# Kernel tuning notes

Hardware: AMD Instinct MI355X
Metric: run time of the kernel (lower is better)

The kernel has to match this reference:

```python
import jax, jax.numpy as jnp
import numpy as np

TOP_K = 2


def setup_inputs() -> dict:
    key = jax.random.key(0)
    ks = jax.random.split(key, 5)
    B, S, H, E, I = 2, 1024, 1024, 16, 1024
    scale = 1.0 / np.sqrt(H)
    return {
        "hidden_states": jax.random.normal(ks[0], (B, S, H), dtype=jnp.float32),
        "router_w": jax.random.normal(ks[1], (E, H), dtype=jnp.float32) * scale,   # nn.Linear(H,E).weight
        "gate_w": jax.random.normal(ks[2], (E, I, H), dtype=jnp.float32) * scale,  # per-expert Linear(H,I).weight
        "up_w": jax.random.normal(ks[3], (E, I, H), dtype=jnp.float32) * scale,
        "down_w": jax.random.normal(ks[4], (E, H, I), dtype=jnp.float32) * (1.0 / np.sqrt(I)),
    }


def reference(hidden_states, router_w, gate_w, up_w, down_w):
    orig_shape = hidden_states.shape
    x = hidden_states.reshape(-1, orig_shape[-1])  # [T, H]
    T = x.shape[0]
    E = router_w.shape[0]

    # Router: sigmoid -> top-k -> normalize
    logits = jnp.einsum("th,eh->te", x, router_w)           # [T, E]
    scores = jax.nn.sigmoid(logits)
    weights, indices = jax.lax.top_k(scores, TOP_K)         # [T, K]
    weights = weights / (weights.sum(axis=-1, keepdims=True) + 1e-20)

    # Dense per-token-per-expert combine weight (0 for unrouted pairs) ==
    # exact math of the torch gather/index_add loop.
    w_full = jnp.zeros((T, E), dtype=x.dtype).at[
        jnp.arange(T)[:, None], indices
    ].add(weights)                                          # [T, E]

    # Expert MLPs (SwiGLU) computed for all experts, zero-weighted combine.
    g = jax.nn.silu(jnp.einsum("th,eih->tei", x, gate_w))   # [T, E, I]
    u = jnp.einsum("th,eih->tei", x, up_w)                  # [T, E, I]
    out = jnp.einsum("te,tei,ehi->th", w_full, g * u, down_w)  # [T, H]
    return out.reshape(orig_shape)
```

## Files before the change

### kernel.cpp

```cpp
#include <hip/hip_runtime.h>
#include <stdint.h>

#define T_TOK 2048
#define H_DIM 1024
#define E_NUM 16
#define I_DIM 1024
#define TOTAL_ROWS (2 * T_TOK)
#define CPAD 16

typedef short bf16x8 __attribute__((ext_vector_type(8)));
typedef float f32x4 __attribute__((ext_vector_type(4)));

__device__ __forceinline__ void async_copy16(const void* g, void* l) {
  __builtin_amdgcn_global_load_lds(
      (const __attribute__((address_space(1))) void*)g,
      (__attribute__((address_space(3))) void*)l, 16, 0, 0);
}

__device__ __forceinline__ uint32_t f2bf(float f) {
  uint32_t u = __float_as_uint(f);
  return (u + 0x7FFFu + ((u >> 16) & 1u)) >> 16;
}
__device__ __forceinline__ uint32_t pk2bf(float lo, float hi) {
  return f2bf(lo) | (f2bf(hi) << 16);
}

__global__ __launch_bounds__(256) void router_kernel(
    const float* __restrict__ x, const float* __restrict__ rw,
    uint16_t* __restrict__ xbf, int* __restrict__ counts,
    int* __restrict__ tokens, float* __restrict__ wts) {
  const int t = blockIdx.x * 4 + (threadIdx.x >> 6);
  const int lane = threadIdx.x & 63;

  float4 xv[4];
  float acc[E_NUM];
#pragma unroll
  for (int e = 0; e < E_NUM; ++e) acc[e] = 0.f;

#pragma unroll
  for (int rep = 0; rep < 4; ++rep) {
    const int h0 = rep * 256 + lane * 4;
    xv[rep] = *(const float4*)(x + (size_t)t * H_DIM + h0);
    uint2 p;
    p.x = pk2bf(xv[rep].x, xv[rep].y);
    p.y = pk2bf(xv[rep].z, xv[rep].w);
    *(uint2*)(xbf + (size_t)t * H_DIM + h0) = p;
  }

#pragma unroll
  for (int e = 0; e < E_NUM; ++e) {
#pragma unroll
    for (int rep = 0; rep < 4; ++rep) {
      const float4 rv = *(const float4*)(rw + (size_t)e * H_DIM + rep * 256 + lane * 4);
      acc[e] += xv[rep].x * rv.x + xv[rep].y * rv.y + xv[rep].z * rv.z +
                xv[rep].w * rv.w;
    }
  }

#pragma unroll
  for (int e = 0; e < E_NUM; ++e) {
    float v = acc[e];
#pragma unroll
    for (int off = 32; off > 0; off >>= 1) v += __shfl_xor(v, off);
    acc[e] = v;
  }

  if (lane < 2) {
    float s[E_NUM];
#pragma unroll
    for (int e = 0; e < E_NUM; ++e) s[e] = 1.f / (1.f + expf(-acc[e]));
    int i1 = 0;
    float v1 = s[0];
#pragma unroll
    for (int e = 1; e < E_NUM; ++e)
      if (s[e] > v1) { v1 = s[e]; i1 = e; }
    int i2 = -1;
    float v2 = -1.f;
#pragma unroll
    for (int e = 0; e < E_NUM; ++e)
      if (e != i1 && s[e] > v2) { v2 = s[e]; i2 = e; }
    const float inv = 1.f / (v1 + v2 + 1e-20f);
    const int pe = (lane == 0) ? i1 : i2;
    const float pw = ((lane == 0) ? v1 : v2) * inv;
    const int slot = atomicAdd(&counts[pe * CPAD], 1);
    tokens[pe * T_TOK + slot] = t;
    wts[pe * T_TOK + slot] = pw;
  }
}

__global__ void offsets_kernel(const int* __restrict__ counts,
                               int* __restrict__ offsets) {
  if (threadIdx.x == 0) {
    int a = 0;
    for (int e = 0; e < E_NUM; ++e) {
      offsets[e] = a;
      a += counts[e * CPAD];
    }
    offsets[E_NUM] = a;
  }
}


__global__ __launch_bounds__(256, 3) void gemm1_kernel(
    const uint16_t* __restrict__ xbf, const float* __restrict__ gate,
    const float* __restrict__ up, const int* __restrict__ counts,
    const int* __restrict__ offsets, const int* __restrict__ tokens,
    const float* __restrict__ wts, uint16_t* __restrict__ hbuf) {
  const int e = blockIdx.z;
  const int count = counts[e * CPAD];
  const int m0 = blockIdx.y * 128;
  if (m0 >= count) return;
  const int n0 = blockIdx.x * 32;

  __shared__ __align__(16) uint16_t As[2][128 * 64];
  __shared__ __align__(16) uint16_t Bgs[2][32 * 64];
  __shared__ __align__(16) uint16_t Bus[2][32 * 64];
  __shared__ int tok_s[128];
  __shared__ float wt_s[128];

  const int tid = threadIdx.x;
  if (tid < 128) {
    const int slot = m0 + tid;
    int tk = 0;
    float w = 0.f;
    if (slot < count) {
      tk = tokens[e * T_TOK + slot];
      w = wts[e * T_TOK + slot];
    }
    tok_s[tid] = tk;
    wt_s[tid] = w;
  }
  __syncthreads();

  const uint16_t* a_g[4];
  int a_c[4];
#pragma unroll
  for (int j = 0; j < 4; ++j) {
    const int c = j * 256 + tid;
    const int m = c >> 3;
    const int kq = (c & 7) ^ (m & 7);
    a_g[j] = xbf + (size_t)tok_s[m] * H_DIM + kq * 8;
    a_c[j] = c * 8;
  }
  const int bm = tid >> 3;
  const int bkq = (tid & 7) ^ (bm & 7);
  const float* g_g = gate + ((size_t)e * I_DIM + n0 + bm) * H_DIM + bkq * 8;
  const float* u_g = up + ((size_t)e * I_DIM + n0 + bm) * H_DIM + bkq * 8;
  const int b_c = tid * 8;

  const int wave = tid >> 6, lane = tid & 63;
  const int wm = wave * 32;
  const int lc = lane & 15, lq = lane >> 4;
  const int l7 = lc & 7;

  f32x4 accg[2][2], accu[2][2];
  const f32x4 zero4 = {0.f, 0.f, 0.f, 0.f};
#pragma unroll
  for (int i = 0; i < 2; ++i)
#pragma unroll
    for (int j = 0; j < 2; ++j) {
      accg[i][j] = zero4;
      accu[i][j] = zero4;
    }

  int am[2], bn[2];
#pragma unroll
  for (int i = 0; i < 2; ++i) am[i] = (wm + i * 16 + lc) * 64;
#pragma unroll
  for (int i = 0; i < 2; ++i) bn[i] = (i * 16 + lc) * 64;

#pragma unroll
  for (int j = 0; j < 4; ++j) async_copy16(a_g[j], &As[0][a_c[j]]);
  float4 g0 = *(const float4*)g_g;
  float4 g1 = *(const float4*)(g_g + 4);
  float4 u0 = *(const float4*)u_g;
  float4 u1 = *(const float4*)(u_g + 4);
  {
    uint4 p;
    p.x = pk2bf(g0.x, g0.y);
    p.y = pk2bf(g0.z, g0.w);
    p.z = pk2bf(g1.x, g1.y);
    p.w = pk2bf(g1.z, g1.w);
    *(uint4*)&Bgs[0][b_c] = p;
    p.x = pk2bf(u0.x, u0.y);
    p.y = pk2bf(u0.z, u0.w);
    p.z = pk2bf(u1.x, u1.y);
    p.w = pk2bf(u1.z, u1.w);
    *(uint4*)&Bus[0][b_c] = p;
  }
  __syncthreads();

  int cur = 0;
  for (int k0 = 0; k0 < H_DIM; k0 += 64) {
    const int nxt = k0 + 64;
    const bool more = (nxt < H_DIM);
    if (more) {
#pragma unroll
      for (int j = 0; j < 4; ++j)
        async_copy16(a_g[j] + nxt, &As[cur ^ 1][a_c[j]]);
      g0 = *(const float4*)(g_g + nxt);
      g1 = *(const float4*)(g_g + nxt + 4);
      u0 = *(const float4*)(u_g + nxt);
      u1 = *(const float4*)(u_g + nxt + 4);
    }

#pragma unroll
    for (int ks = 0; ks < 2; ++ks) {
      const int kswz = ((ks * 4 + lq) ^ l7) * 8;
      bf16x8 af[2], bg[2], bu[2];
#pragma unroll
      for (int i = 0; i < 2; ++i)
        af[i] = *(const bf16x8*)&As[cur][am[i] + kswz];
#pragma unroll
      for (int i = 0; i < 2; ++i) {
        bg[i] = *(const bf16x8*)&Bgs[cur][bn[i] + kswz];
        bu[i] = *(const bf16x8*)&Bus[cur][bn[i] + kswz];
      }
#pragma unroll
      for (int im = 0; im < 2; ++im)
#pragma unroll
        for (int in = 0; in < 2; ++in) {
          accg[im][in] = __builtin_amdgcn_mfma_f32_16x16x32_bf16(
              af[im], bg[in], accg[im][in], 0, 0, 0);
          accu[im][in] = __builtin_amdgcn_mfma_f32_16x16x32_bf16(
              af[im], bu[in], accu[im][in], 0, 0, 0);
        }
    }

    if (more) {
      uint4 p;
      p.x = pk2bf(g0.x, g0.y);
      p.y = pk2bf(g0.z, g0.w);
      p.z = pk2bf(g1.x, g1.y);
      p.w = pk2bf(g1.z, g1.w);
      *(uint4*)&Bgs[cur ^ 1][b_c] = p;
      p.x = pk2bf(u0.x, u0.y);
      p.y = pk2bf(u0.z, u0.w);
      p.z = pk2bf(u1.x, u1.y);
      p.w = pk2bf(u1.z, u1.w);
      *(uint4*)&Bus[cur ^ 1][b_c] = p;
      __syncthreads();
      cur ^= 1;
    }
  }

  const int off_e = offsets[e];
#pragma unroll
  for (int im = 0; im < 2; ++im) {
#pragma unroll
    for (int r = 0; r < 4; ++r) {
      const int row = wm + im * 16 + lq * 4 + r;
      const int slot = m0 + row;
      if (slot < count) {
        const float w = wt_s[row];
        uint16_t* hrow = hbuf + (size_t)(off_e + slot) * I_DIM + n0;
#pragma unroll
        for (int in = 0; in < 2; ++in) {
          const float g = accg[im][in][r];
          const float u = accu[im][in][r];
          const float hv = g / (1.f + __expf(-g)) * u * w;
          hrow[in * 16 + lc] = (uint16_t)f2bf(hv);
        }
      }
    }
  }
}

__global__ __launch_bounds__(256, 3) void gemm2_kernel(
    const uint16_t* __restrict__ hbuf, const float* __restrict__ down,
    const int* __restrict__ counts, const int* __restrict__ offsets,
    const int* __restrict__ tokens, float* __restrict__ out) {
  const int e = blockIdx.z;
  const int count = counts[e * CPAD];
  const int m0 = blockIdx.y * 128;
  if (m0 >= count) return;
  const int n0 = blockIdx.x * 32;

  __shared__ __align__(16) uint16_t As[2][128 * 64];
  __shared__ __align__(16) uint16_t Bs[2][32 * 64];
  __shared__ int tok_s[128];

  const int tid = threadIdx.x;
  const int off_e = offsets[e];
  if (tid < 128) {
    const int slot = m0 + tid;
    tok_s[tid] = (slot < count) ? tokens[e * T_TOK + slot] : 0;
  }

  const uint16_t* a_g[4];
  int a_c[4];
#pragma unroll
  for (int j = 0; j < 4; ++j) {
    const int c = j * 256 + tid;
    const int m = c >> 3;
    const int kq = (c & 7) ^ (m & 7);
    int r = off_e + m0 + m;
    if (r > TOTAL_ROWS - 1) r = TOTAL_ROWS - 1;
    a_g[j] = hbuf + (size_t)r * I_DIM + kq * 8;
    a_c[j] = c * 8;
  }
  const int bm = tid >> 3;
  const int bkq = (tid & 7) ^ (bm & 7);
  const float* d_g = down + ((size_t)e * H_DIM + n0 + bm) * I_DIM + bkq * 8;
  const int b_c = tid * 8;

  const int wave = tid >> 6, lane = tid & 63;
  const int wm = wave * 32;
  const int lc = lane & 15, lq = lane >> 4;
  const int l7 = lc & 7;

  f32x4 acc[2][2];
  const f32x4 zero4 = {0.f, 0.f, 0.f, 0.f};
#pragma unroll
  for (int i = 0; i < 2; ++i)
#pragma unroll
    for (int j = 0; j < 2; ++j) acc[i][j] = zero4;

  int am[2], bn[2];
#pragma unroll
  for (int i = 0; i < 2; ++i) am[i] = (wm + i * 16 + lc) * 64;
#pragma unroll
  for (int i = 0; i < 2; ++i) bn[i] = (i * 16 + lc) * 64;

#pragma unroll
  for (int j = 0; j < 4; ++j) async_copy16(a_g[j], &As[0][a_c[j]]);
  float4 d0 = *(const float4*)d_g;
  float4 d1 = *(const float4*)(d_g + 4);
  {
    uint4 p;
    p.x = pk2bf(d0.x, d0.y);
    p.y = pk2bf(d0.z, d0.w);
    p.z = pk2bf(d1.x, d1.y);
    p.w = pk2bf(d1.z, d1.w);
    *(uint4*)&Bs[0][b_c] = p;
  }
  __syncthreads();

  int cur = 0;
  for (int k0 = 0; k0 < I_DIM; k0 += 64) {
    const int nxt = k0 + 64;
    const bool more = (nxt < I_DIM);
    if (more) {
#pragma unroll
      for (int j = 0; j < 4; ++j)
        async_copy16(a_g[j] + nxt, &As[cur ^ 1][a_c[j]]);
      d0 = *(const float4*)(d_g + nxt);
      d1 = *(const float4*)(d_g + nxt + 4);
    }

#pragma unroll
    for (int ks = 0; ks < 2; ++ks) {
      const int kswz = ((ks * 4 + lq) ^ l7) * 8;
      bf16x8 af[2], bf[2];
#pragma unroll
      for (int i = 0; i < 2; ++i)
        af[i] = *(const bf16x8*)&As[cur][am[i] + kswz];
#pragma unroll
      for (int i = 0; i < 2; ++i)
        bf[i] = *(const bf16x8*)&Bs[cur][bn[i] + kswz];
#pragma unroll
      for (int im = 0; im < 2; ++im)
#pragma unroll
        for (int in = 0; in < 2; ++in)
          acc[im][in] = __builtin_amdgcn_mfma_f32_16x16x32_bf16(
              af[im], bf[in], acc[im][in], 0, 0, 0);
    }

    if (more) {
      uint4 p;
      p.x = pk2bf(d0.x, d0.y);
      p.y = pk2bf(d0.z, d0.w);
      p.z = pk2bf(d1.x, d1.y);
      p.w = pk2bf(d1.z, d1.w);
      *(uint4*)&Bs[cur ^ 1][b_c] = p;
      __syncthreads();
      cur ^= 1;
    }
  }

#pragma unroll
  for (int im = 0; im < 2; ++im) {
#pragma unroll
    for (int r = 0; r < 4; ++r) {
      const int row = wm + im * 16 + lq * 4 + r;
      const int slot = m0 + row;
      if (slot < count) {
        float* orow = out + (size_t)tok_s[row] * H_DIM + n0;
#pragma unroll
        for (int in = 0; in < 2; ++in)
          atomicAdd(orow + in * 16 + lc, acc[im][in][r]);
      }
    }
  }
}

extern "C" void kernel_launch(void* const* d_in, const int* in_sizes, int n_in,
                              void* d_out, int out_size, void* d_ws,
                              size_t ws_size, hipStream_t stream) {
  const float* x = (const float*)d_in[0];
  const float* rw = (const float*)d_in[1];
  const float* gate = (const float*)d_in[2];
  const float* up = (const float*)d_in[3];
  const float* down = (const float*)d_in[4];
  float* out = (float*)d_out;

  uint8_t* ws = (uint8_t*)d_ws;
  int* counts = (int*)ws;
  int* offsets = (int*)(ws + 2048);
  int* tokens = (int*)(ws + 4096);
  float* wts = (float*)(ws + 4096 + 131072);
  uint16_t* xbf = (uint16_t*)(ws + 4096 + 262144);
  uint16_t* hbuf = (uint16_t*)(ws + 4096 + 262144 + 4194304);

  hipMemsetAsync(counts, 0, 2048, stream);
  hipMemsetAsync(out, 0, (size_t)out_size * sizeof(float), stream);

  router_kernel<<<512, 256, 0, stream>>>(x, rw, xbf, counts, tokens, wts);
  offsets_kernel<<<1, 64, 0, stream>>>(counts, offsets);
  gemm1_kernel<<<dim3(32, 16, 16), 256, 0, stream>>>(
      xbf, gate, up, counts, offsets, tokens, wts, hbuf);
  gemm2_kernel<<<dim3(32, 16, 16), 256, 0, stream>>>(hbuf, down, counts,
                                                     offsets, tokens, out);
}
```

Before: 299.5 us.

## Pre-convert expert weights to swizzled bf16 tiles before grouped GEMMs

Adds a prep phase to the router kernel that converts gate, up and down weights from fp32 to bf16 in a tiled, XOR-swizzled layout in workspace. The GEMM kernels then stream the bf16 tiles with async LDS copies and use wider 64-column N tiles, so expert weights no longer need in-kernel fp32 loading and conversion. The cost is an extra full pass over all weights each call (reading 192MB of fp32 and writing 96MB of bf16). It also needs about 100MB more workspace and falls back to the old kernels when that space is not available.

```diff
diff --git a/kernel.cpp b/kernel.cpp
--- a/kernel.cpp
+++ b/kernel.cpp
@@ -25,66 +25,114 @@
   return f2bf(lo) | (f2bf(hi) << 16);
 }
 
-__global__ __launch_bounds__(256) void router_kernel(
+#define WS_COUNTS 0
+#define WS_OFFSETS 2048
+#define WS_TOKENS 4096
+#define WS_WTS (4096 + 131072)
+#define WS_XBF (4096 + 262144)
+#define WS_HBUF (WS_XBF + 4194304)
+#define WS_GBUF (WS_HBUF + 8388608)
+#define WS_UBUF (WS_GBUF + 33554432)
+#define WS_DBUF (WS_UBUF + 33554432)
+#define WS_NEED (WS_DBUF + 33554432)
+
+__global__ __launch_bounds__(256) void router_prep_kernel(
     const float* __restrict__ x, const float* __restrict__ rw,
-    uint16_t* __restrict__ xbf, int* __restrict__ counts,
-    int* __restrict__ tokens, float* __restrict__ wts) {
-  const int t = blockIdx.x * 4 + (threadIdx.x >> 6);
-  const int lane = threadIdx.x & 63;
-
-  float4 xv[4];
-  float acc[E_NUM];
-#pragma unroll
-  for (int e = 0; e < E_NUM; ++e) acc[e] = 0.f;
-
-#pragma unroll
-  for (int rep = 0; rep < 4; ++rep) {
-    const int h0 = rep * 256 + lane * 4;
-    xv[rep] = *(const float4*)(x + (size_t)t * H_DIM + h0);
-    uint2 p;
-    p.x = pk2bf(xv[rep].x, xv[rep].y);
-    p.y = pk2bf(xv[rep].z, xv[rep].w);
-    *(uint2*)(xbf + (size_t)t * H_DIM + h0) = p;
-  }
-
-#pragma unroll
-  for (int e = 0; e < E_NUM; ++e) {
+    const float* __restrict__ gate, const float* __restrict__ up,
+    const float* __restrict__ down, uint16_t* __restrict__ xbf,
+    int* __restrict__ counts, int* __restrict__ tokens,
+    float* __restrict__ wts, uint16_t* __restrict__ gbuf,
+    uint16_t* __restrict__ ubuf, uint16_t* __restrict__ dbuf) {
+  const int bid = blockIdx.x;
+  const int tid = threadIdx.x;
+
+  if (bid < 512) {
+    const int t = bid * 4 + (tid >> 6);
+    const int lane = tid & 63;
+
+    float4 xv[4];
+    float acc[E_NUM];
+#pragma unroll
+    for (int e = 0; e < E_NUM; ++e) acc[e] = 0.f;
+
 #pragma unroll
     for (int rep = 0; rep < 4; ++rep) {
-      const float4 rv = *(const float4*)(rw + (size_t)e * H_DIM + rep * 256 + lane * 4);
-      acc[e] += xv[rep].x * rv.x + xv[rep].y * rv.y + xv[rep].z * rv.z +
-                xv[rep].w * rv.w;
-    }
-  }
-
-#pragma unroll
-  for (int e = 0; e < E_NUM; ++e) {
-    float v = acc[e];
-#pragma unroll
-    for (int off = 32; off > 0; off >>= 1) v += __shfl_xor(v, off);
-    acc[e] = v;
-  }
-
-  if (lane < 2) {
-    float s[E_NUM];
-#pragma unroll
-    for (int e = 0; e < E_NUM; ++e) s[e] = 1.f / (1.f + expf(-acc[e]));
-    int i1 = 0;
-    float v1 = s[0];
-#pragma unroll
-    for (int e = 1; e < E_NUM; ++e)
-      if (s[e] > v1) { v1 = s[e]; i1 = e; }
-    int i2 = -1;
-    float v2 = -1.f;
-#pragma unroll
-    for (int e = 0; e < E_NUM; ++e)
-      if (e != i1 && s[e] > v2) { v2 = s[e]; i2 = e; }
-    const float inv = 1.f / (v1 + v2 + 1e-20f);
-    const int pe = (lane == 0) ? i1 : i2;
-    const float pw = ((lane == 0) ? v1 : v2) * inv;
-    const int slot = atomicAdd(&counts[pe * CPAD], 1);
-    tokens[pe * T_TOK + slot] = t;
-    wts[pe * T_TOK + slot] = pw;
+      const int h0 = rep * 256 + lane * 4;
+      xv[rep] = *(const float4*)(x + (size_t)t * H_DIM + h0);
+      uint2 p;
+      p.x = pk2bf(xv[rep].x, xv[rep].y);
+      p.y = pk2bf(xv[rep].z, xv[rep].w);
+      *(uint2*)(xbf + (size_t)t * H_DIM + h0) = p;
+    }
+
+#pragma unroll
+    for (int e = 0; e < E_NUM; ++e) {
+#pragma unroll
+      for (int rep = 0; rep < 4; ++rep) {
+        const float4 rv =
+            *(const float4*)(rw + (size_t)e * H_DIM + rep * 256 + lane * 4);
+        acc[e] += xv[rep].x * rv.x + xv[rep].y * rv.y + xv[rep].z * rv.z +
+                  xv[rep].w * rv.w;
+      }
+    }
+
+#pragma unroll
+    for (int e = 0; e < E_NUM; ++e) {
+      float v = acc[e];
+#pragma unroll
+      for (int off = 32; off > 0; off >>= 1) v += __shfl_xor(v, off);
+      acc[e] = v;
+    }
+
+    if (lane < 2) {
+      float s[E_NUM];
+#pragma unroll
+      for (int e = 0; e < E_NUM; ++e) s[e] = 1.f / (1.f + expf(-acc[e]));
+      int i1 = 0;
+      float v1 = s[0];
+#pragma unroll
+      for (int e = 1; e < E_NUM; ++e)
+        if (s[e] > v1) { v1 = s[e]; i1 = e; }
+      int i2 = -1;
+      float v2 = -1.f;
+#pragma unroll
+      for (int e = 0; e < E_NUM; ++e)
+        if (e != i1 && s[e] > v2) { v2 = s[e]; i2 = e; }
+      const float inv = 1.f / (v1 + v2 + 1e-20f);
+      const int pe = (lane == 0) ? i1 : i2;
+      const float pw = ((lane == 0) ? v1 : v2) * inv;
+      const int slot = atomicAdd(&counts[pe * CPAD], 1);
+      tokens[pe * T_TOK + slot] = t;
+      wts[pe * T_TOK + slot] = pw;
+    }
+    return;
+  }
+
+  const int tt = bid - 512;
+  const int mat = tt >> 12;
+  const int r = tt & 4095;
+  const int e = r >> 8;
+  const int nt = (r >> 4) & 15;
+  const int kt = r & 15;
+  const float* W = (mat == 0) ? gate : (mat == 1) ? up : down;
+  uint16_t* D = (mat == 0) ? gbuf : (mat == 1) ? ubuf : dbuf;
+  const float* src = W + ((size_t)e * 1024 + (size_t)nt * 64) * 1024 + kt * 64;
+  uint16_t* dst = D + ((size_t)((e * 16 + nt) * 16 + kt)) * 4096;
+
+#pragma unroll
+  for (int h = 0; h < 2; ++h) {
+    const int c = tid + h * 256;
+    const int m = c >> 3;
+    const int kq = (c & 7) ^ (m & 7);
+    const float* s = src + (size_t)m * 1024 + kq * 8;
+    const float4 a = *(const float4*)s;
+    const float4 b = *(const float4*)(s + 4);
+    uint4 p;
+    p.x = pk2bf(a.x, a.y);
+    p.y = pk2bf(a.z, a.w);
+    p.z = pk2bf(b.x, b.y);
+    p.w = pk2bf(b.z, b.w);
+    *(uint4*)(dst + (size_t)c * 8) = p;
   }
 }
 
@@ -100,8 +148,262 @@
   }
 }
 
-
-__global__ __launch_bounds__(256, 3) void gemm1_kernel(
+__global__ __launch_bounds__(256, 2) void gemm1_kernel(
+    const uint16_t* __restrict__ xbf, const uint16_t* __restrict__ gbuf,
+    const uint16_t* __restrict__ ubuf, const int* __restrict__ counts,
+    const int* __restrict__ offsets, const int* __restrict__ tokens,
+    const float* __restrict__ wts, uint16_t* __restrict__ hbuf) {
+  const int e = blockIdx.z;
+  const int count = counts[e * CPAD];
+  const int m0 = blockIdx.y * 128;
+  if (m0 >= count) return;
+  const int n0t = blockIdx.x;
+
+  __shared__ __align__(16) uint16_t As[2][128 * 64];
+  __shared__ __align__(16) uint16_t Bgs[2][64 * 64];
+  __shared__ __align__(16) uint16_t Bus[2][64 * 64];
+  __shared__ int tok_s[128];
+  __shared__ float wt_s[128];
+
+  const int tid = threadIdx.x;
+  if (tid < 128) {
+    const int slot = m0 + tid;
+    int tk = 0;
+    float w = 0.f;
+    if (slot < count) {
+      tk = tokens[e * T_TOK + slot];
+      w = wts[e * T_TOK + slot];
+    }
+    tok_s[tid] = tk;
+    wt_s[tid] = w;
+  }
+  __syncthreads();
+
+  const uint16_t* a_g[4];
+  int a_c[4];
+#pragma unroll
+  for (int j = 0; j < 4; ++j) {
+    const int c = j * 256 + tid;
+    const int m = c >> 3;
+    const int kq = (c & 7) ^ (m & 7);
+    a_g[j] = xbf + (size_t)tok_s[m] * H_DIM + kq * 8;
+    a_c[j] = c * 8;
+  }
+  const uint16_t* g_g = gbuf + (size_t)((e * 16 + n0t) * 16) * 4096;
+  const uint16_t* u_g = ubuf + (size_t)((e * 16 + n0t) * 16) * 4096;
+  const int bc0 = tid * 8, bc1 = (tid + 256) * 8;
+
+  const int wave = tid >> 6, lane = tid & 63;
+  const int wm = wave * 32;
+  const int lc = lane & 15, lq = lane >> 4;
+  const int l7 = lc & 7;
+
+  f32x4 accg[2][4], accu[2][4];
+  const f32x4 zero4 = {0.f, 0.f, 0.f, 0.f};
+#pragma unroll
+  for (int i = 0; i < 2; ++i)
+#pragma unroll
+    for (int j = 0; j < 4; ++j) {
+      accg[i][j] = zero4;
+      accu[i][j] = zero4;
+    }
+
+  int am[2], bn[4];
+#pragma unroll
+  for (int i = 0; i < 2; ++i) am[i] = (wm + i * 16 + lc) * 64;
+#pragma unroll
+  for (int i = 0; i < 4; ++i) bn[i] = (i * 16 + lc) * 64;
+
+#pragma unroll
+  for (int j = 0; j < 4; ++j) async_copy16(a_g[j], &As[0][a_c[j]]);
+  async_copy16(g_g + bc0, &Bgs[0][bc0]);
+  async_copy16(g_g + bc1, &Bgs[0][bc1]);
+  async_copy16(u_g + bc0, &Bus[0][bc0]);
+  async_copy16(u_g + bc1, &Bus[0][bc1]);
+  __syncthreads();
+
+  int cur = 0;
+  for (int kt = 0; kt < 16; ++kt) {
+    const bool more = (kt < 15);
+    if (more) {
+      const int ko = (kt + 1) * 64;
+      const int bo = (kt + 1) * 4096;
+      const int nb = cur ^ 1;
+#pragma unroll
+      for (int j = 0; j < 4; ++j) async_copy16(a_g[j] + ko, &As[nb][a_c[j]]);
+      async_copy16(g_g + bo + bc0, &Bgs[nb][bc0]);
+      async_copy16(g_g + bo + bc1, &Bgs[nb][bc1]);
+      async_copy16(u_g + bo + bc0, &Bus[nb][bc0]);
+      async_copy16(u_g + bo + bc1, &Bus[nb][bc1]);
+    }
+
+#pragma unroll
+    for (int ks = 0; ks < 2; ++ks) {
+      const int kswz = ((ks * 4 + lq) ^ l7) * 8;
+      bf16x8 af[2], bg[4], bu[4];
+#pragma unroll
+      for (int i = 0; i < 2; ++i)
+        af[i] = *(const bf16x8*)&As[cur][am[i] + kswz];
+#pragma unroll
+      for (int i = 0; i < 4; ++i) {
+        bg[i] = *(const bf16x8*)&Bgs[cur][bn[i] + kswz];
+        bu[i] = *(const bf16x8*)&Bus[cur][bn[i] + kswz];
+      }
+#pragma unroll
+      for (int im = 0; im < 2; ++im)
+#pragma unroll
+        for (int in = 0; in < 4; ++in) {
+          accg[im][in] = __builtin_amdgcn_mfma_f32_16x16x32_bf16(
+              af[im], bg[in], accg[im][in], 0, 0, 0);
+          accu[im][in] = __builtin_amdgcn_mfma_f32_16x16x32_bf16(
+              af[im], bu[in], accu[im][in], 0, 0, 0);
+        }
+    }
+
+    if (more) {
+      __syncthreads();
+      cur ^= 1;
+    }
+  }
+
+  const int off_e = offsets[e];
+#pragma unroll
+  for (int im = 0; im < 2; ++im) {
+#pragma unroll
+    for (int r = 0; r < 4; ++r) {
+      const int row = wm + im * 16 + lq * 4 + r;
+      const int slot = m0 + row;
+      if (slot < count) {
+        const float w = wt_s[row];
+        uint16_t* hrow = hbuf + (size_t)(off_e + slot) * I_DIM + n0t * 64;
+#pragma unroll
+        for (int in = 0; in < 4; ++in) {
+          const float g = accg[im][in][r];
+          const float u = accu[im][in][r];
+          const float hv = g / (1.f + __expf(-g)) * u * w;
+          hrow[in * 16 + lc] = (uint16_t)f2bf(hv);
+        }
+      }
+    }
+  }
+}
+
+__global__ __launch_bounds__(256, 3) void gemm2_kernel(
+    const uint16_t* __restrict__ hbuf, const uint16_t* __restrict__ dbuf,
+    const int* __restrict__ counts, const int* __restrict__ offsets,
+    const int* __restrict__ tokens, float* __restrict__ out) {
+  const int e = blockIdx.z;
+  const int count = counts[e * CPAD];
+  const int m0 = blockIdx.y * 128;
+  if (m0 >= count) return;
+  const int n0t = blockIdx.x;
+
+  __shared__ __align__(16) uint16_t As[2][128 * 64];
+  __shared__ __align__(16) uint16_t Bs[2][64 * 64];
+  __shared__ int tok_s[128];
+
+  const int tid = threadIdx.x;
+  const int off_e = offsets[e];
+  if (tid < 128) {
+    const int slot = m0 + tid;
+    tok_s[tid] = (slot < count) ? tokens[e * T_TOK + slot] : 0;
+  }
+
+  const uint16_t* a_g[4];
+  int a_c[4];
+#pragma unroll
+  for (int j = 0; j < 4; ++j) {
+    const int c = j * 256 + tid;
+    const int m = c >> 3;
+    const int kq = (c & 7) ^ (m & 7);
+    int r = off_e + m0 + m;
+    if (r > TOTAL_ROWS - 1) r = TOTAL_ROWS - 1;
+    a_g[j] = hbuf + (size_t)r * I_DIM + kq * 8;
+    a_c[j] = c * 8;
+  }
+  const uint16_t* d_g = dbuf + (size_t)((e * 16 + n0t) * 16) * 4096;
+  const int bc0 = tid * 8, bc1 = (tid + 256) * 8;
+
+  const int wave = tid >> 6, lane = tid & 63;
+  const int wm = wave * 32;
+  const int lc = lane & 15, lq = lane >> 4;
+  const int l7 = lc & 7;
+
+  f32x4 acc[2][4];
+  const f32x4 zero4 = {0.f, 0.f, 0.f, 0.f};
+#pragma unroll
+  for (int i = 0; i < 2; ++i)
+#pragma unroll
+    for (int j = 0; j < 4; ++j) acc[i][j] = zero4;
+
+  int am[2], bn[4];
+#pragma unroll
+  for (int i = 0; i < 2; ++i) am[i] = (wm + i * 16 + lc) * 64;
+#pragma unroll
+  for (int i = 0; i < 4; ++i) bn[i] = (i * 16 + lc) * 64;
+
+  __syncthreads();
+
+#pragma unroll
+  for (int j = 0; j < 4; ++j) async_copy16(a_g[j], &As[0][a_c[j]]);
+  async_copy16(d_g + bc0, &Bs[0][bc0]);
+  async_copy16(d_g + bc1, &Bs[0][bc1]);
+  __syncthreads();
+
+  int cur = 0;
+  for (int kt = 0; kt < 16; ++kt) {
+    const bool more = (kt < 15);
+    if (more) {
+      const int ko = (kt + 1) * 64;
+      const int bo = (kt + 1) * 4096;
+      const int nb = cur ^ 1;
+#pragma unroll
+      for (int j = 0; j < 4; ++j) async_copy16(a_g[j] + ko, &As[nb][a_c[j]]);
+      async_copy16(d_g + bo + bc0, &Bs[nb][bc0]);
+      async_copy16(d_g + bo + bc1, &Bs[nb][bc1]);
+    }
+
+#pragma unroll
+    for (int ks = 0; ks < 2; ++ks) {
+      const int kswz = ((ks * 4 + lq) ^ l7) * 8;
+      bf16x8 af[2], bf[4];
+#pragma unroll
+      for (int i = 0; i < 2; ++i)
+        af[i] = *(const bf16x8*)&As[cur][am[i] + kswz];
+#pragma unroll
+      for (int i = 0; i < 4; ++i)
+        bf[i] = *(const bf16x8*)&Bs[cur][bn[i] + kswz];
+#pragma unroll
+      for (int im = 0; im < 2; ++im)
+#pragma unroll
+        for (int in = 0; in < 4; ++in)
+          acc[im][in] = __builtin_amdgcn_mfma_f32_16x16x32_bf16(
+              af[im], bf[in], acc[im][in], 0, 0, 0);
+    }
+
+    if (more) {
+      __syncthreads();
+      cur ^= 1;
+    }
+  }
+
+#pragma unroll
+  for (int im = 0; im < 2; ++im) {
+#pragma unroll
+    for (int r = 0; r < 4; ++r) {
+      const int row = wm + im * 16 + lq * 4 + r;
+      const int slot = m0 + row;
+      if (slot < count) {
+        float* orow = out + (size_t)tok_s[row] * H_DIM + n0t * 64;
+#pragma unroll
+        for (int in = 0; in < 4; ++in)
+          atomicAdd(orow + in * 16 + lc, acc[im][in][r]);
+      }
+    }
+  }
+}
+
+__global__ __launch_bounds__(256, 3) void gemm1_fb(
     const uint16_t* __restrict__ xbf, const float* __restrict__ gate,
     const float* __restrict__ up, const int* __restrict__ counts,
     const int* __restrict__ offsets, const int* __restrict__ tokens,
@@ -266,7 +568,7 @@
   }
 }
 
-__global__ __launch_bounds__(256, 3) void gemm2_kernel(
+__global__ __launch_bounds__(256, 3) void gemm2_fb(
     const uint16_t* __restrict__ hbuf, const float* __restrict__ down,
     const int* __restrict__ counts, const int* __restrict__ offsets,
     const int* __restrict__ tokens, float* __restrict__ out) {
@@ -405,20 +707,36 @@
   float* out = (float*)d_out;
 
   uint8_t* ws = (uint8_t*)d_ws;
-  int* counts = (int*)ws;
-  int* offsets = (int*)(ws + 2048);
-  int* tokens = (int*)(ws + 4096);
-  float* wts = (float*)(ws + 4096 + 131072);
-  uint16_t* xbf = (uint16_t*)(ws + 4096 + 262144);
-  uint16_t* hbuf = (uint16_t*)(ws + 4096 + 262144 + 4194304);
+  int* counts = (int*)(ws + WS_COUNTS);
+  int* offsets = (int*)(ws + WS_OFFSETS);
+  int* tokens = (int*)(ws + WS_TOKENS);
+  float* wts = (float*)(ws + WS_WTS);
+  uint16_t* xbf = (uint16_t*)(ws + WS_XBF);
+  uint16_t* hbuf = (uint16_t*)(ws + WS_HBUF);
+  uint16_t* gbuf = (uint16_t*)(ws + WS_GBUF);
+  uint16_t* ubuf = (uint16_t*)(ws + WS_UBUF);
+  uint16_t* dbuf = (uint16_t*)(ws + WS_DBUF);
+
+  const bool big = (ws_size >= (size_t)WS_NEED);
 
   hipMemsetAsync(counts, 0, 2048, stream);
   hipMemsetAsync(out, 0, (size_t)out_size * sizeof(float), stream);
 
-  router_kernel<<<512, 256, 0, stream>>>(x, rw, xbf, counts, tokens, wts);
-  offsets_kernel<<<1, 64, 0, stream>>>(counts, offsets);
-  gemm1_kernel<<<dim3(32, 16, 16), 256, 0, stream>>>(
-      xbf, gate, up, counts, offsets, tokens, wts, hbuf);
-  gemm2_kernel<<<dim3(32, 16, 16), 256, 0, stream>>>(hbuf, down, counts,
-                                                     offsets, tokens, out);
-}
+  if (big) {
+    router_prep_kernel<<<512 + 12288, 256, 0, stream>>>(
+        x, rw, gate, up, down, xbf, counts, tokens, wts, gbuf, ubuf, dbuf);
+    offsets_kernel<<<1, 64, 0, stream>>>(counts, offsets);
+    gemm1_kernel<<<dim3(16, 16, 16), 256, 0, stream>>>(
+        xbf, gbuf, ubuf, counts, offsets, tokens, wts, hbuf);
+    gemm2_kernel<<<dim3(16, 16, 16), 256, 0, stream>>>(hbuf, dbuf, counts,
+                                                       offsets, tokens, out);
+  } else {
+    router_prep_kernel<<<512, 256, 0, stream>>>(
+        x, rw, gate, up, down, xbf, counts, tokens, wts, gbuf, ubuf, dbuf);
+    offsets_kernel<<<1, 64, 0, stream>>>(counts, offsets);
+    gemm1_fb<<<dim3(32, 16, 16), 256, 0, stream>>>(
+        xbf, gate, up, counts, offsets, tokens, wts, hbuf);
+    gemm2_fb<<<dim3(32, 16, 16), 256, 0, stream>>>(hbuf, down, counts,
+                                                   offsets, tokens, out);
+  }
+}
```

After: 303.6 us. Within noise of the previous version (+1.4%).
